# Optimization experiments

Measured on AMD Instinct MI355X. Metric: run time of the kernel, lower is better.

Reference implementation:

```python
import jax, jax.numpy as jnp
import numpy as np
from jax import lax

B, T = 64, 2048
D_LSTM, D_ENC, D_ATT, N_F, K = 1024, 512, 128, 32, 31
PAD = (K - 1) // 2  # 15, 'same' padding as Tacotron2 LocationLayer


def setup_inputs() -> dict:
    key = jax.random.key(0)
    ks = jax.random.split(key, 11)
    def w(k, shape, fan_in):
        return jax.random.normal(k, shape, dtype=jnp.float32) / np.sqrt(fan_in)
    return {
        "query": jax.random.normal(ks[0], (B, 1, D_LSTM), dtype=jnp.float32),
        "memory": jax.random.normal(ks[1], (B, T, D_ENC), dtype=jnp.float32),
        "attention_weights_cat": jax.random.uniform(ks[2], (B, 2, T), dtype=jnp.float32),
        "Wq": w(ks[3], (D_ATT, D_LSTM), D_LSTM),
        "bq": jnp.zeros((D_ATT,), jnp.float32),
        "Wm": w(ks[4], (D_ATT, D_ENC), D_ENC),
        "bm": jnp.zeros((D_ATT,), jnp.float32),
        "Wconv": w(ks[5], (N_F, 2, K), 2 * K),  # Conv1d weight [out, in, k], bias=False
        "Wloc": w(ks[6], (D_ATT, N_F), N_F),     # location dense, bias=False
        "Wv": w(ks[7], (1, D_ATT), D_ATT),
        "bv": jnp.zeros((1,), jnp.float32),
    }


def reference(query, memory, attention_weights_cat, Wq, bq, Wm, bm, Wconv, Wloc, Wv, bv):
    # query_layer: [B,1,D_LSTM] -> [B,1,D_ATT]
    q = query @ Wq.T + bq
    # memory_layer: [B,T,D_ENC] -> [B,T,D_ATT]
    k = memory @ Wm.T + bm
    # location_layer: Conv1d same-pad over time, then dense to D_ATT
    conv = lax.conv_general_dilated(
        attention_weights_cat, Wconv, window_strides=(1,),
        padding=[(PAD, PAD)], dimension_numbers=("NCH", "OIH", "NCH"))  # [B,N_F,T]
    loc = jnp.einsum("bft,af->bta", conv, Wloc)  # [B,T,D_ATT]
    # energies: v^T tanh(q + k + loc) -> [B,T]
    energies = (jnp.tanh(q + k + loc) @ Wv.T + bv).squeeze(-1)
    attention_weights = jax.nn.softmax(energies, axis=1)  # [B,T]
    attention_context = jnp.einsum("bt,btd->bd", attention_weights, memory)  # [B,D_ENC]
    return attention_context, attention_weights
```

## Files before the change

### kernel.cpp

```cpp
#include <hip/hip_runtime.h>
#include <math.h>

#define B_ 64
#define T_ 2048
#define DL 1024
#define DE 512
#define DA 128
#define NF 32
#define KW 31
#define PADW 15
#define TT 128
#define LDA 40

typedef short bf16x8 __attribute__((ext_vector_type(8)));
typedef float f32x4 __attribute__((ext_vector_type(4)));

__device__ __forceinline__ void split_bf16(float x, unsigned short &hi, unsigned short &lo) {
    unsigned u = __float_as_uint(x);
    unsigned short h = (unsigned short)((u + 0x7FFFu + ((u >> 16) & 1u)) >> 16);
    float hf = __uint_as_float((unsigned)h << 16);
    float l = x - hf;
    unsigned ul = __float_as_uint(l);
    hi = h;
    lo = (unsigned short)((ul + 0x7FFFu + ((ul >> 16) & 1u)) >> 16);
}

__device__ __forceinline__ float fast_tanh(float x) {
    x = fminf(fmaxf(x, -15.f), 15.f);
    float e2 = __expf(2.f * x);
    return (e2 - 1.f) * __builtin_amdgcn_rcpf(e2 + 1.f);
}

__global__ __launch_bounds__(256) void prep_kernel(const float* __restrict__ Wm,
                                                   const float* __restrict__ Wloc,
                                                   unsigned short* __restrict__ bg_hi,
                                                   unsigned short* __restrict__ bg_lo,
                                                   unsigned short* __restrict__ bw_hi,
                                                   unsigned short* __restrict__ bw_lo) {
    int i = blockIdx.x * 256 + threadIdx.x;
    unsigned short h, l;
    if (i < DA * DE) {
        split_bf16(Wm[i], h, l);
        bg_hi[i] = h;
        bg_lo[i] = l;
    } else {
        int j = i - DA * DE;
        split_bf16(Wloc[j], h, l);
        bw_hi[j] = h;
        bw_lo[j] = l;
    }
}

__global__ __launch_bounds__(128) void q_kernel(const float* __restrict__ query,
                                                const float* __restrict__ Wq,
                                                const float* __restrict__ bq,
                                                float* __restrict__ qbuf) {
    int b = blockIdx.x;
    int a = threadIdx.x;
    __shared__ __align__(16) float qs[DL];
    for (int i = threadIdx.x; i < DL; i += 128) qs[i] = query[(size_t)b * DL + i];
    __syncthreads();
    const float* wrow = Wq + (size_t)a * DL;
    float acc = 0.f;
#pragma unroll 8
    for (int i = 0; i < DL; i += 4) {
        float4 w = *(const float4*)(wrow + i);
        float4 q4 = *(const float4*)(qs + i);
        acc += w.x * q4.x + w.y * q4.y + w.z * q4.z + w.w * q4.w;
    }
    qbuf[(size_t)b * DA + a] = acc + bq[a];
}

__global__ __launch_bounds__(256, 2) void energy_kernel(
    const float* __restrict__ mem,
    const float* __restrict__ attw,
    const unsigned short* __restrict__ bg_hi,
    const unsigned short* __restrict__ bg_lo,
    const unsigned short* __restrict__ bw_hi,
    const unsigned short* __restrict__ bw_lo,
    const float* __restrict__ bm,
    const float* __restrict__ Wconv,
    const float* __restrict__ Wv,
    const float* __restrict__ bv,
    const float* __restrict__ qbuf,
    float* __restrict__ e_out)
{
    __shared__ __align__(16) unsigned short Ahi[TT * LDA];
    __shared__ __align__(16) unsigned short Alo[TT * LDA];
    __shared__ __align__(16) unsigned short Bhi[DA * LDA];
    __shared__ __align__(16) unsigned short Blo[DA * LDA];
    __shared__ __align__(16) float attw_s[2 * 160];
    __shared__ __align__(16) float wconv_s[NF * 64];
    __shared__ float qb_s[DA], wv_s[DA];
    __shared__ float e_part[2][TT];

    const int tid = threadIdx.x;
    const int b = blockIdx.y;
    const int t0 = blockIdx.x * TT;
    const int lane = tid & 63;
    const int wave = tid >> 6;
    const int wm = wave & 1, wn = wave >> 1;
    const int m = lane & 15;
    const int q8 = (lane >> 4) * 8;

    if (tid < DA) {
        qb_s[tid] = qbuf[(size_t)b * DA + tid] + bm[tid];
        wv_s[tid] = Wv[tid];
    }

    for (int i = tid; i < 2 * (TT + KW - 1); i += 256) {
        int c = i / 158, j = i % 158;
        int t = t0 - PADW + j;
        attw_s[c * 160 + j] = (t >= 0 && t < T_) ? attw[((size_t)b * 2 + c) * T_ + t] : 0.f;
    }
    for (int i = tid; i < NF * 2 * KW; i += 256) {
        int f = i / 62, r = i % 62;
        wconv_s[f * 64 + r] = Wconv[i];
    }
    __syncthreads();

    for (int i = tid; i < TT * NF; i += 256) {
        int t = i >> 5, f = i & 31;
        const float* w0 = wconv_s + f * 64;
        const float* a0 = attw_s + t;
        const float* a1 = attw_s + 160 + t;
        float s = 0.f;
#pragma unroll
        for (int k = 0; k < KW; ++k) s += w0[k] * a0[k] + w0[31 + k] * a1[k];
        unsigned short h, l;
        split_bf16(s, h, l);
        Ahi[t * LDA + f] = h;
        Alo[t * LDA + f] = l;
    }
#pragma unroll
    for (int r = 0; r < 2; ++r) {
        int idx = tid + 256 * r;
        int a = idx >> 2, c8 = (idx & 3) * 8;
        *(uint4*)(Bhi + a * LDA + c8) = *(const uint4*)(bw_hi + a * NF + c8);
        *(uint4*)(Blo + a * LDA + c8) = *(const uint4*)(bw_lo + a * NF + c8);
    }
    __syncthreads();

    f32x4 acc[4][4];
#pragma unroll
    for (int mi = 0; mi < 4; ++mi)
#pragma unroll
        for (int ni = 0; ni < 4; ++ni) {
            f32x4 z = {0.f, 0.f, 0.f, 0.f};
            acc[mi][ni] = z;
        }

    auto mfma_step = [&]() {
        bf16x8 ah[4], al[4], bh[4], bl[4];
#pragma unroll
        for (int mi = 0; mi < 4; ++mi) {
            int r = (wm * 64 + mi * 16 + m) * LDA + q8;
            ah[mi] = *(const bf16x8*)(Ahi + r);
            al[mi] = *(const bf16x8*)(Alo + r);
        }
#pragma unroll
        for (int ni = 0; ni < 4; ++ni) {
            int r = (wn * 64 + ni * 16 + m) * LDA + q8;
            bh[ni] = *(const bf16x8*)(Bhi + r);
            bl[ni] = *(const bf16x8*)(Blo + r);
        }
        __builtin_amdgcn_s_setprio(1);
#pragma unroll
        for (int ni = 0; ni < 4; ++ni)
#pragma unroll
            for (int mi = 0; mi < 4; ++mi)
                acc[mi][ni] = __builtin_amdgcn_mfma_f32_16x16x32_bf16(ah[mi], bh[ni], acc[mi][ni], 0, 0, 0);
#pragma unroll
        for (int ni = 0; ni < 4; ++ni)
#pragma unroll
            for (int mi = 0; mi < 4; ++mi)
                acc[mi][ni] = __builtin_amdgcn_mfma_f32_16x16x32_bf16(ah[mi], bl[ni], acc[mi][ni], 0, 0, 0);
#pragma unroll
        for (int ni = 0; ni < 4; ++ni)
#pragma unroll
            for (int mi = 0; mi < 4; ++mi)
                acc[mi][ni] = __builtin_amdgcn_mfma_f32_16x16x32_bf16(al[mi], bh[ni], acc[mi][ni], 0, 0, 0);
        __builtin_amdgcn_s_setprio(0);
    };

    const size_t mem_base = ((size_t)b * T_ + t0) * DE;

    float4 rA[4];
#pragma unroll
    for (int r = 0; r < 4; ++r) {
        int idx = tid + 256 * r;
        int t = idx >> 3, c4 = (idx & 7) * 4;
        rA[r] = *(const float4*)(mem + mem_base + (size_t)t * DE + c4);
    }

    mfma_step();

#pragma unroll 1
    for (int c = 0; c < 16; ++c) {
        const int k0 = c * 32;
        asm volatile("s_barrier" ::: "memory");
        uint4 rbh[2], rbl[2];
#pragma unroll
        for (int r = 0; r < 2; ++r) {
            int idx = tid + 256 * r;
            int a = idx >> 2, c8 = (idx & 3) * 8;
            rbh[r] = *(const uint4*)(bg_hi + (size_t)a * DE + k0 + c8);
            rbl[r] = *(const uint4*)(bg_lo + (size_t)a * DE + k0 + c8);
        }
#pragma unroll
        for (int r = 0; r < 4; ++r) {
            int idx = tid + 256 * r;
            int t = idx >> 3, c4 = (idx & 7) * 4;
            unsigned short h0, l0, h1, l1, h2, l2, h3, l3;
            split_bf16(rA[r].x, h0, l0);
            split_bf16(rA[r].y, h1, l1);
            split_bf16(rA[r].z, h2, l2);
            split_bf16(rA[r].w, h3, l3);
            ushort4 hv = {h0, h1, h2, h3};
            ushort4 lv = {l0, l1, l2, l3};
            *(ushort4*)(Ahi + t * LDA + c4) = hv;
            *(ushort4*)(Alo + t * LDA + c4) = lv;
        }
#pragma unroll
        for (int r = 0; r < 2; ++r) {
            int idx = tid + 256 * r;
            int a = idx >> 2, c8 = (idx & 3) * 8;
            *(uint4*)(Bhi + a * LDA + c8) = rbh[r];
            *(uint4*)(Blo + a * LDA + c8) = rbl[r];
        }
        if (c < 15) {
            const int k0n = k0 + 32;
#pragma unroll
            for (int r = 0; r < 4; ++r) {
                int idx = tid + 256 * r;
                int t = idx >> 3, c4 = (idx & 7) * 4;
                rA[r] = *(const float4*)(mem + mem_base + (size_t)t * DE + k0n + c4);
            }
        }
        asm volatile("s_waitcnt lgkmcnt(0)\n\ts_barrier" ::: "memory");
        mfma_step();
    }

    float wvr[4], qbr[4];
#pragma unroll
    for (int ni = 0; ni < 4; ++ni) {
        int a = wn * 64 + ni * 16 + m;
        wvr[ni] = wv_s[a];
        qbr[ni] = qb_s[a];
    }
    float bvv = bv[0];
#pragma unroll
    for (int mi = 0; mi < 4; ++mi) {
#pragma unroll
        for (int reg = 0; reg < 4; ++reg) {
            float s = 0.f;
#pragma unroll
            for (int ni = 0; ni < 4; ++ni)
                s += wvr[ni] * fast_tanh(acc[mi][ni][reg] + qbr[ni]);
            s += __shfl_xor(s, 1, 64);
            s += __shfl_xor(s, 2, 64);
            s += __shfl_xor(s, 4, 64);
            s += __shfl_xor(s, 8, 64);
            if (m == 0)
                e_part[wn][wm * 64 + mi * 16 + (lane >> 4) * 4 + reg] = s;
        }
    }
    __syncthreads();
    if (tid < TT)
        e_out[(size_t)b * T_ + t0 + tid] = e_part[0][tid] + e_part[1][tid] + bvv;
}

__global__ __launch_bounds__(256) void softmax_kernel(const float* __restrict__ e,
                                                      float* __restrict__ wout) {
    int b = blockIdx.x;
    int tid = threadIdx.x;
    __shared__ float red[4];
    float v[8];
    float m = -1e30f;
#pragma unroll
    for (int r = 0; r < 8; ++r) {
        v[r] = e[(size_t)b * T_ + r * 256 + tid];
        m = fmaxf(m, v[r]);
    }
#pragma unroll
    for (int off = 1; off < 64; off <<= 1) m = fmaxf(m, __shfl_xor(m, off, 64));
    if ((tid & 63) == 0) red[tid >> 6] = m;
    __syncthreads();
    m = fmaxf(fmaxf(red[0], red[1]), fmaxf(red[2], red[3]));
    __syncthreads();
    float s = 0.f;
#pragma unroll
    for (int r = 0; r < 8; ++r) {
        v[r] = expf(v[r] - m);
        s += v[r];
    }
#pragma unroll
    for (int off = 1; off < 64; off <<= 1) s += __shfl_xor(s, off, 64);
    if ((tid & 63) == 0) red[tid >> 6] = s;
    __syncthreads();
    s = red[0] + red[1] + red[2] + red[3];
    float inv = 1.0f / s;
#pragma unroll
    for (int r = 0; r < 8; ++r) wout[(size_t)b * T_ + r * 256 + tid] = v[r] * inv;
}

__global__ __launch_bounds__(256) void ctx_partial_kernel(const float* __restrict__ mem,
                                                          const float* __restrict__ w,
                                                          float* __restrict__ partial) {
    int b = blockIdx.y, tc = blockIdx.x;
    int tid = threadIdx.x;
    __shared__ float ws_s[128];
    __shared__ float red[512];
    if (tid < 128) ws_s[tid] = w[(size_t)b * T_ + tc * 128 + tid];
    __syncthreads();
    int d = (tid & 127) * 4;
    int th = tid >> 7;
    const float* mp = mem + ((size_t)b * T_ + tc * 128 + th * 64) * DE + d;
    float a0 = 0.f, a1 = 0.f, a2 = 0.f, a3 = 0.f;
#pragma unroll 8
    for (int t = 0; t < 64; ++t) {
        float4 v = *(const float4*)(mp + (size_t)t * DE);
        float wv = ws_s[th * 64 + t];
        a0 += wv * v.x; a1 += wv * v.y; a2 += wv * v.z; a3 += wv * v.w;
    }
    if (th == 1) {
        float* r = red + (tid & 127) * 4;
        r[0] = a0; r[1] = a1; r[2] = a2; r[3] = a3;
    }
    __syncthreads();
    if (th == 0) {
        const float* r = red + tid * 4;
        float* pp = partial + ((size_t)b * 16 + tc) * DE + d;
        pp[0] = a0 + r[0]; pp[1] = a1 + r[1]; pp[2] = a2 + r[2]; pp[3] = a3 + r[3];
    }
}

__global__ __launch_bounds__(512) void ctx_reduce_kernel(const float* __restrict__ partial,
                                                         float* __restrict__ ctx) {
    int b = blockIdx.x;
    int d = threadIdx.x;
    float s = 0.f;
#pragma unroll
    for (int j = 0; j < 16; ++j) s += partial[((size_t)b * 16 + j) * DE + d];
    ctx[(size_t)b * DE + d] = s;
}

extern "C" void kernel_launch(void* const* d_in, const int* in_sizes, int n_in,
                              void* d_out, int out_size, void* d_ws, size_t ws_size,
                              hipStream_t stream) {
    const float* query  = (const float*)d_in[0];
    const float* memory = (const float*)d_in[1];
    const float* attw   = (const float*)d_in[2];
    const float* Wq     = (const float*)d_in[3];
    const float* bq     = (const float*)d_in[4];
    const float* Wm     = (const float*)d_in[5];
    const float* bm     = (const float*)d_in[6];
    const float* Wconv  = (const float*)d_in[7];
    const float* Wloc   = (const float*)d_in[8];
    const float* Wv     = (const float*)d_in[9];
    const float* bv     = (const float*)d_in[10];

    float* out = (float*)d_out;
    float* ctx_out = out;
    float* w_out = out + B_ * DE;

    float* ws = (float*)d_ws;
    float* qbuf = ws;
    float* ebuf = qbuf + B_ * DA;
    float* partial = ebuf + (size_t)B_ * T_;
    unsigned short* bg_hi = (unsigned short*)(partial + (size_t)B_ * 16 * DE);
    unsigned short* bg_lo = bg_hi + DA * DE;
    unsigned short* bw_hi = bg_lo + DA * DE;
    unsigned short* bw_lo = bw_hi + DA * NF;

    prep_kernel<<<dim3((DA * DE + DA * NF) / 256), dim3(256), 0, stream>>>(
        Wm, Wloc, bg_hi, bg_lo, bw_hi, bw_lo);
    q_kernel<<<dim3(B_), dim3(128), 0, stream>>>(query, Wq, bq, qbuf);
    energy_kernel<<<dim3(T_ / TT, B_), dim3(256), 0, stream>>>(
        memory, attw, bg_hi, bg_lo, bw_hi, bw_lo, bm, Wconv, Wv, bv, qbuf, ebuf);
    softmax_kernel<<<dim3(B_), dim3(256), 0, stream>>>(ebuf, w_out);
    ctx_partial_kernel<<<dim3(16, B_), dim3(256), 0, stream>>>(memory, w_out, partial);
    ctx_reduce_kernel<<<dim3(B_), dim3(512), 0, stream>>>(partial, ctx_out);
}
```

Baseline: 513.4 us.

## Fuse context accumulation into energy kernel using per-chunk online softmax

The energy kernel now computes a local max and sum of exponentials over its 128-step chunk and accumulates an unnormalised partial context from the memory tile while it is likely still in cache. A combined softmax/context kernel rescales the 16 chunk partials with the global max and sum. This removes a second full pass over memory and two kernel launches, at the cost of more work and register pressure in the energy kernel; launch bounds are also raised to 3 blocks per CU. It relies on a mem_base variable defined in the unseen part of the kernel.

```diff
diff --git a/kernel.cpp b/kernel.cpp
--- a/kernel.cpp
+++ b/kernel.cpp
@@ -71,7 +71,7 @@
     qbuf[(size_t)b * DA + a] = acc + bq[a];
 }
 
-__global__ __launch_bounds__(256, 2) void energy_kernel(
+__global__ __launch_bounds__(256, 3) void energy_kernel(
     const float* __restrict__ mem,
     const float* __restrict__ attw,
     const unsigned short* __restrict__ bg_hi,
@@ -83,7 +83,9 @@
     const float* __restrict__ Wv,
     const float* __restrict__ bv,
     const float* __restrict__ qbuf,
-    float* __restrict__ e_out)
+    float* __restrict__ e_out,
+    float* __restrict__ pctx,
+    float* __restrict__ msbuf)
 {
     __shared__ __align__(16) unsigned short Ahi[TT * LDA];
     __shared__ __align__(16) unsigned short Alo[TT * LDA];
@@ -96,7 +98,8 @@
 
     const int tid = threadIdx.x;
     const int b = blockIdx.y;
-    const int t0 = blockIdx.x * TT;
+    const int tc = blockIdx.x;
+    const int t0 = tc * TT;
     const int lane = tid & 63;
     const int wave = tid >> 6;
     const int wm = wave & 1, wn = wave >> 1;
@@ -266,15 +269,58 @@
         }
     }
     __syncthreads();
-    if (tid < TT)
-        e_out[(size_t)b * T_ + t0 + tid] = e_part[0][tid] + e_part[1][tid] + bvv;
-}
-
-__global__ __launch_bounds__(256) void softmax_kernel(const float* __restrict__ e,
-                                                      float* __restrict__ wout) {
+
+    float ee = -1e30f;
+    if (tid < TT) {
+        ee = e_part[0][tid] + e_part[1][tid] + bvv;
+        e_out[(size_t)b * T_ + t0 + tid] = ee;
+    }
+    float* redf = attw_s;
+    float* p_s = wconv_s;
+    float mx = ee;
+#pragma unroll
+    for (int off = 32; off >= 1; off >>= 1) mx = fmaxf(mx, __shfl_xor(mx, off, 64));
+    if (lane == 0) redf[wave] = mx;
+    __syncthreads();
+    const float m_loc = fmaxf(fmaxf(redf[0], redf[1]), fmaxf(redf[2], redf[3]));
+    float pt = 0.f;
+    if (tid < TT) {
+        pt = __expf(ee - m_loc);
+        p_s[tid] = pt;
+    }
+    float ss = pt;
+#pragma unroll
+    for (int off = 32; off >= 1; off >>= 1) ss += __shfl_xor(ss, off, 64);
+    if (lane == 0) redf[8 + wave] = ss;
+    __syncthreads();
+    if (tid == 0) {
+        const float s_loc = redf[8] + redf[9] + redf[10] + redf[11];
+        msbuf[((size_t)b * 16 + tc) * 2 + 0] = m_loc;
+        msbuf[((size_t)b * 16 + tc) * 2 + 1] = s_loc;
+    }
+    const int d0 = tid * 2;
+    const float* mp = mem + mem_base + d0;
+    float c0 = 0.f, c1 = 0.f;
+#pragma unroll 8
+    for (int t = 0; t < TT; ++t) {
+        float pv = p_s[t];
+        float2 v = *(const float2*)(mp + (size_t)t * DE);
+        c0 += pv * v.x;
+        c1 += pv * v.y;
+    }
+    float2 cv = {c0, c1};
+    *(float2*)(pctx + ((size_t)b * 16 + tc) * DE + d0) = cv;
+}
+
+__global__ __launch_bounds__(256) void softmax_ctx_kernel(const float* __restrict__ e,
+                                                          const float* __restrict__ msbuf,
+                                                          const float* __restrict__ pctx,
+                                                          float* __restrict__ wout,
+                                                          float* __restrict__ ctx) {
     int b = blockIdx.x;
     int tid = threadIdx.x;
     __shared__ float red[4];
+    __shared__ float scl[16];
     float v[8];
     float m = -1e30f;
 #pragma unroll
@@ -302,47 +348,29 @@
     float inv = 1.0f / s;
 #pragma unroll
     for (int r = 0; r < 8; ++r) wout[(size_t)b * T_ + r * 256 + tid] = v[r] * inv;
-}
-
-__global__ __launch_bounds__(256) void ctx_partial_kernel(const float* __restrict__ mem,
-                                                          const float* __restrict__ w,
-                                                          float* __restrict__ partial) {
-    int b = blockIdx.y, tc = blockIdx.x;
-    int tid = threadIdx.x;
-    __shared__ float ws_s[128];
-    __shared__ float red[512];
-    if (tid < 128) ws_s[tid] = w[(size_t)b * T_ + tc * 128 + tid];
-    __syncthreads();
-    int d = (tid & 127) * 4;
-    int th = tid >> 7;
-    const float* mp = mem + ((size_t)b * T_ + tc * 128 + th * 64) * DE + d;
-    float a0 = 0.f, a1 = 0.f, a2 = 0.f, a3 = 0.f;
-#pragma unroll 8
-    for (int t = 0; t < 64; ++t) {
-        float4 v = *(const float4*)(mp + (size_t)t * DE);
-        float wv = ws_s[th * 64 + t];
-        a0 += wv * v.x; a1 += wv * v.y; a2 += wv * v.z; a3 += wv * v.w;
-    }
-    if (th == 1) {
-        float* r = red + (tid & 127) * 4;
-        r[0] = a0; r[1] = a1; r[2] = a2; r[3] = a3;
-    }
-    __syncthreads();
-    if (th == 0) {
-        const float* r = red + tid * 4;
-        float* pp = partial + ((size_t)b * 16 + tc) * DE + d;
-        pp[0] = a0 + r[0]; pp[1] = a1 + r[1]; pp[2] = a2 + r[2]; pp[3] = a3 + r[3];
-    }
-}
-
-__global__ __launch_bounds__(512) void ctx_reduce_kernel(const float* __restrict__ partial,
-                                                         float* __restrict__ ctx) {
-    int b = blockIdx.x;
-    int d = threadIdx.x;
-    float s = 0.f;
-#pragma unroll
-    for (int j = 0; j < 16; ++j) s += partial[((size_t)b * 16 + j) * DE + d];
-    ctx[(size_t)b * DE + d] = s;
+
+    float mj = (tid < 16) ? msbuf[((size_t)b * 16 + tid) * 2 + 0] : -1e30f;
+    float sj = (tid < 16) ? msbuf[((size_t)b * 16 + tid) * 2 + 1] : 0.f;
+    float M = mj;
+#pragma unroll
+    for (int off = 8; off >= 1; off >>= 1) M = fmaxf(M, __shfl_xor(M, off, 64));
+    float sc = sj * __expf(mj - M);
+    float S = sc;
+#pragma unroll
+    for (int off = 8; off >= 1; off >>= 1) S += __shfl_xor(S, off, 64);
+    if (tid < 16) scl[tid] = __expf(mj - M) / S;
+    __syncthreads();
+    const int d0 = tid * 2;
+    float c0 = 0.f, c1 = 0.f;
+#pragma unroll
+    for (int j = 0; j < 16; ++j) {
+        float sv = scl[j];
+        float2 pv = *(const float2*)(pctx + ((size_t)b * 16 + j) * DE + d0);
+        c0 += sv * pv.x;
+        c1 += sv * pv.y;
+    }
+    float2 cv = {c0, c1};
+    *(float2*)(ctx + (size_t)b * DE + d0) = cv;
 }
 
 extern "C" void kernel_launch(void* const* d_in, const int* in_sizes, int n_in,
@@ -367,8 +395,9 @@
     float* ws = (float*)d_ws;
     float* qbuf = ws;
     float* ebuf = qbuf + B_ * DA;
-    float* partial = ebuf + (size_t)B_ * T_;
-    unsigned short* bg_hi = (unsigned short*)(partial + (size_t)B_ * 16 * DE);
+    float* pctx = ebuf + (size_t)B_ * T_;
+    float* msbuf = pctx + (size_t)B_ * 16 * DE;
+    unsigned short* bg_hi = (unsigned short*)(msbuf + B_ * 16 * 2);
     unsigned short* bg_lo = bg_hi + DA * DE;
     unsigned short* bw_hi = bg_lo + DA * DE;
     unsigned short* bw_lo = bw_hi + DA * NF;
@@ -377,8 +406,7 @@
         Wm, Wloc, bg_hi, bg_lo, bw_hi, bw_lo);
     q_kernel<<<dim3(B_), dim3(128), 0, stream>>>(query, Wq, bq, qbuf);
     energy_kernel<<<dim3(T_ / TT, B_), dim3(256), 0, stream>>>(
-        memory, attw, bg_hi, bg_lo, bw_hi, bw_lo, bm, Wconv, Wv, bv, qbuf, ebuf);
-    softmax_kernel<<<dim3(B_), dim3(256), 0, stream>>>(ebuf, w_out);
-    ctx_partial_kernel<<<dim3(16, B_), dim3(256), 0, stream>>>(memory, w_out, partial);
-    ctx_reduce_kernel<<<dim3(B_), dim3(512), 0, stream>>>(partial, ctx_out);
-}
+        memory, attw, bg_hi, bg_lo, bw_hi, bw_lo, bm, Wconv, Wv, bv, qbuf,
+        ebuf, pctx, msbuf);
+    softmax_ctx_kernel<<<dim3(B_), dim3(256), 0, stream>>>(ebuf, msbuf, pctx, w_out, ctx_out);
+}
```

Result: slower. 541.4 us (+5.5%).
